# Kernel optimization log

Hardware: AMD Instinct MI355X
Metric: run time of the kernel (lower is better)

Reference implementation:

```python
import jax, jax.numpy as jnp
import numpy as np
import math

T, E = 8192, 64            # tokens, experts
K_VALUE = 2                # top-2 router
CAP_FACTOR = 1.25          # capacity_factor_train (module in training mode)
MIN_CAPACITY = 4


def _get_capacity(tokens, experts):
    cap = math.floor(K_VALUE * CAP_FACTOR * tokens / experts)
    cap += cap % 2  # make even
    cap = max(cap, MIN_CAPACITY)
    assert cap > 0
    return int(cap)


def setup_inputs() -> dict:
    key = jax.random.key(0)
    inputs = jax.random.normal(key, (T, E), dtype=jnp.float32)
    return {"inputs": inputs}


def reference(inputs):
    tokens, experts = inputs.shape
    capacity = _get_capacity(tokens, experts)  # static (shape-derived)

    probs = jax.nn.softmax(inputs, axis=-1)                       # [T, E]
    top1_idx = jnp.argmax(probs, axis=-1)                         # [T]
    mask1 = jax.nn.one_hot(top1_idx, experts, dtype=jnp.int32)    # [T, E]
    probs_except1 = jnp.where(mask1.astype(bool), -jnp.inf, probs)
    top2_idx = jnp.argmax(probs_except1, axis=-1)                 # [T]
    mask2 = jax.nn.one_hot(top2_idx, experts, dtype=jnp.int32)

    # position of each token in its expert's queue (moe_cumsum = cumsum - 1)
    rank1 = jnp.cumsum(mask1, axis=0) - 1                          # [T, E]
    rank2 = jnp.cumsum(mask2, axis=0) - 1 + jnp.sum(mask1, axis=0, keepdims=True)

    # drop tokens beyond capacity
    mask1 = mask1 * (rank1 < capacity)
    mask2 = mask2 * (rank2 < capacity)
    used_capacity = mask1.sum(axis=0) + mask2.sum(axis=0)          # [E]

    # per-token slot index (0 if dropped) and gate weight (0 if dropped)
    r1 = jnp.sum(mask1 * rank1, axis=-1)                           # [T]
    r2 = jnp.sum(mask2 * rank2, axis=-1)
    w1 = jnp.sum(mask1 * probs, axis=-1)                           # [T]
    w2 = jnp.sum(mask2 * probs, axis=-1)
    m1b = jnp.sum(mask1, axis=-1).astype(bool)                     # kept flags
    m2b = jnp.sum(mask2, axis=-1).astype(bool)

    idx = jnp.arange(tokens)
    cb_weight = jnp.zeros((tokens, experts, capacity), dtype=inputs.dtype)
    cb_weight = cb_weight.at[idx, top1_idx, r1].add(w1)
    cb_weight = cb_weight.at[idx, top2_idx, r2].add(w2)

    sec_mask = jnp.zeros((tokens, experts, capacity), dtype=bool)
    sec_mask = sec_mask.at[idx, top1_idx, r1].max(m1b)
    sec_mask = sec_mask.at[idx, top2_idx, r2].max(m2b)

    return used_capacity, cb_weight, sec_mask
```

## Files before the change

### kernel.cpp

```cpp
#include <hip/hip_runtime.h>
#include <hip/hip_bf16.h>
#include <math.h>

#define T_TOKENS 8192
#define N_EXP    64
#define CAP      320
#define ROWSZ    (N_EXP * CAP)

__global__ __launch_bounds__(256) void moe_topk_kernel(
    const float* __restrict__ in,
    int* __restrict__ top1, int* __restrict__ top2,
    float* __restrict__ w1, float* __restrict__ w2)
{
    const int lane = threadIdx.x & 63;
    const int wv   = threadIdx.x >> 6;
    const int g    = lane >> 4;
    const int sub  = lane & 15;
    const int t    = blockIdx.x * 16 + wv * 4 + g;

    const float4 xv = ((const float4*)in)[(size_t)t * 16 + sub];
    const int b0 = sub * 4;

    float v = xv.x; int idx = b0;
    if (xv.y > v) { v = xv.y; idx = b0 + 1; }
    if (xv.z > v) { v = xv.z; idx = b0 + 2; }
    if (xv.w > v) { v = xv.w; idx = b0 + 3; }
    #pragma unroll
    for (int off = 8; off; off >>= 1) {
        float vo = __shfl_xor(v, off);
        int   io = __shfl_xor(idx, off);
        if (vo > v || (vo == v && io < idx)) { v = vo; idx = io; }
    }
    const float m  = v;
    const int   i1 = idx;

    float s = expf(xv.x - m) + expf(xv.y - m) + expf(xv.z - m) + expf(xv.w - m);
    #pragma unroll
    for (int off = 8; off; off >>= 1) s += __shfl_xor(s, off);

    const float c0 = (b0     == i1) ? -INFINITY : xv.x;
    const float c1 = (b0 + 1 == i1) ? -INFINITY : xv.y;
    const float c2 = (b0 + 2 == i1) ? -INFINITY : xv.z;
    const float c3 = (b0 + 3 == i1) ? -INFINITY : xv.w;
    float v2 = c0; int idx2 = b0;
    if (c1 > v2) { v2 = c1; idx2 = b0 + 1; }
    if (c2 > v2) { v2 = c2; idx2 = b0 + 2; }
    if (c3 > v2) { v2 = c3; idx2 = b0 + 3; }
    #pragma unroll
    for (int off = 8; off; off >>= 1) {
        float vo = __shfl_xor(v2, off);
        int   io = __shfl_xor(idx2, off);
        if (vo > v2 || (vo == v2 && io < idx2)) { v2 = vo; idx2 = io; }
    }

    if (sub == 0) {
        top1[t] = i1;
        top2[t] = idx2;
        w1[t]   = 1.0f / s;
        w2[t]   = expf(v2 - m) / s;
    }
}

__global__ __launch_bounds__(1024) void moe_rank_scatter_kernel(
    const int* __restrict__ top1, const int* __restrict__ top2,
    const float* __restrict__ w1, const float* __restrict__ w2,
    float* __restrict__ out)
{
    const int e    = blockIdx.x;
    const int tid  = threadIdx.x;
    const int lane = tid & 63;
    const int wid  = tid >> 6;

    __shared__ int wsA[16], wsB[16];

    float* __restrict__ cb  = out + N_EXP;
    float* __restrict__ sec = cb + (size_t)T_TOKENS * ROWSZ;

    const int4 a1 = ((const int4*)top1)[tid * 2];
    const int4 b1 = ((const int4*)top1)[tid * 2 + 1];
    const int m0 = (a1.x == e), m1 = (a1.y == e), m2 = (a1.z == e), m3 = (a1.w == e);
    const int m4 = (b1.x == e), m5 = (b1.y == e), m6 = (b1.z == e), m7 = (b1.w == e);
    const int cnt1 = m0 + m1 + m2 + m3 + m4 + m5 + m6 + m7;

    int sc = cnt1;
    #pragma unroll
    for (int off = 1; off < 64; off <<= 1) {
        int n = __shfl_up(sc, off);
        if (lane >= off) sc += n;
    }
    if (lane == 63) wsA[wid] = sc;
    __syncthreads();
    int wbase = 0, total1 = 0;
    #pragma unroll
    for (int w = 0; w < 16; ++w) {
        const int sv = wsA[w];
        if (w < wid) wbase += sv;
        total1 += sv;
    }
    {
        int r = wbase + sc - cnt1;
        const int t0 = tid * 8;
        #define SCAT1(K, MK)                                                  \
            if (MK) {                                                         \
                if (r < CAP) {                                                \
                    const size_t o = (size_t)(t0 + K) * ROWSZ + e * CAP + r;  \
                    cb[o]  = w1[t0 + K];                                      \
                    sec[o] = 1.0f;                                            \
                }                                                             \
                ++r;                                                          \
            }
        SCAT1(0, m0) SCAT1(1, m1) SCAT1(2, m2) SCAT1(3, m3)
        SCAT1(4, m4) SCAT1(5, m5) SCAT1(6, m6) SCAT1(7, m7)
        #undef SCAT1
    }

    const int4 a2 = ((const int4*)top2)[tid * 2];
    const int4 b2 = ((const int4*)top2)[tid * 2 + 1];
    const int n0 = (a2.x == e), n1 = (a2.y == e), n2 = (a2.z == e), n3 = (a2.w == e);
    const int n4 = (b2.x == e), n5 = (b2.y == e), n6 = (b2.z == e), n7 = (b2.w == e);
    const int cnt2 = n0 + n1 + n2 + n3 + n4 + n5 + n6 + n7;

    int sc2 = cnt2;
    #pragma unroll
    for (int off = 1; off < 64; off <<= 1) {
        int n = __shfl_up(sc2, off);
        if (lane >= off) sc2 += n;
    }
    if (lane == 63) wsB[wid] = sc2;
    __syncthreads();
    int wbase2 = 0, total2 = 0;
    #pragma unroll
    for (int w = 0; w < 16; ++w) {
        const int sv = wsB[w];
        if (w < wid) wbase2 += sv;
        total2 += sv;
    }
    {
        int r = total1 + wbase2 + sc2 - cnt2;
        const int t0 = tid * 8;
        #define SCAT2(K, NK)                                                  \
            if (NK) {                                                         \
                if (r < CAP) {                                                \
                    const size_t o = (size_t)(t0 + K) * ROWSZ + e * CAP + r;  \
                    cb[o]  = w2[t0 + K];                                      \
                    sec[o] = 1.0f;                                            \
                }                                                             \
                ++r;                                                          \
            }
        SCAT2(0, n0) SCAT2(1, n1) SCAT2(2, n2) SCAT2(3, n3)
        SCAT2(4, n4) SCAT2(5, n5) SCAT2(6, n6) SCAT2(7, n7)
        #undef SCAT2
    }

    if (tid == 0) {
        const int kept1 = min(total1, CAP);
        const int kept2 = min(max(CAP - total1, 0), total2);
        out[e] = (float)(kept1 + kept2);
    }
}

extern "C" void kernel_launch(void* const* d_in, const int* in_sizes, int n_in,
                              void* d_out, int out_size, void* d_ws, size_t ws_size,
                              hipStream_t stream) {
    const float* in  = (const float*)d_in[0];
    float*       out = (float*)d_out;

    int*   top1 = (int*)d_ws;
    int*   top2 = top1 + T_TOKENS;
    float* w1   = (float*)(top2 + T_TOKENS);
    float* w2   = w1 + T_TOKENS;

    hipMemsetAsync(d_out, 0, (size_t)out_size * sizeof(float), stream);

    moe_topk_kernel<<<T_TOKENS / 16, 256, 0, stream>>>(in, top1, top2, w1, w2);
    moe_rank_scatter_kernel<<<N_EXP, 1024, 0, stream>>>(top1, top2, w1, w2, out);
}
```

Before: 231.4 us.

## Replace memset and sparse scatter with a dense vectorized fill kernel

```diff
diff --git a/kernel.cpp b/kernel.cpp
--- a/kernel.cpp
+++ b/kernel.cpp
@@ -6,11 +6,15 @@
 #define N_EXP    64
 #define CAP      320
 #define ROWSZ    (N_EXP * CAP)
+#define ROWQ     (ROWSZ / 4)
+#define CBQ4     ((unsigned)(T_TOKENS) * (unsigned)ROWQ)
+
+typedef float f32x4 __attribute__((ext_vector_type(4)));
 
 __global__ __launch_bounds__(256) void moe_topk_kernel(
     const float* __restrict__ in,
     int* __restrict__ top1, int* __restrict__ top2,
-    float* __restrict__ w1, float* __restrict__ w2)
+    float2* __restrict__ wp)
 {
     const int lane = threadIdx.x & 63;
     const int wv   = threadIdx.x >> 6;
@@ -39,13 +43,13 @@
     for (int off = 8; off; off >>= 1) s += __shfl_xor(s, off);
 
     const float c0 = (b0     == i1) ? -INFINITY : xv.x;
-    const float c1 = (b0 + 1 == i1) ? -INFINITY : xv.y;
-    const float c2 = (b0 + 2 == i1) ? -INFINITY : xv.z;
-    const float c3 = (b0 + 3 == i1) ? -INFINITY : xv.w;
+    const float c1v = (b0 + 1 == i1) ? -INFINITY : xv.y;
+    const float c2v = (b0 + 2 == i1) ? -INFINITY : xv.z;
+    const float c3v = (b0 + 3 == i1) ? -INFINITY : xv.w;
     float v2 = c0; int idx2 = b0;
-    if (c1 > v2) { v2 = c1; idx2 = b0 + 1; }
-    if (c2 > v2) { v2 = c2; idx2 = b0 + 2; }
-    if (c3 > v2) { v2 = c3; idx2 = b0 + 3; }
+    if (c1v > v2) { v2 = c1v; idx2 = b0 + 1; }
+    if (c2v > v2) { v2 = c2v; idx2 = b0 + 2; }
+    if (c3v > v2) { v2 = c3v; idx2 = b0 + 3; }
     #pragma unroll
     for (int off = 8; off; off >>= 1) {
         float vo = __shfl_xor(v2, off);
@@ -56,14 +60,13 @@
     if (sub == 0) {
         top1[t] = i1;
         top2[t] = idx2;
-        w1[t]   = 1.0f / s;
-        w2[t]   = expf(v2 - m) / s;
+        wp[t]   = make_float2(1.0f / s, expf(v2 - m) / s);
     }
 }
 
-__global__ __launch_bounds__(1024) void moe_rank_scatter_kernel(
+__global__ __launch_bounds__(1024) void moe_rank_kernel(
     const int* __restrict__ top1, const int* __restrict__ top2,
-    const float* __restrict__ w1, const float* __restrict__ w2,
+    int* __restrict__ c1, int* __restrict__ c2,
     float* __restrict__ out)
 {
     const int e    = blockIdx.x;
@@ -72,9 +75,6 @@
     const int wid  = tid >> 6;
 
     __shared__ int wsA[16], wsB[16];
-
-    float* __restrict__ cb  = out + N_EXP;
-    float* __restrict__ sec = cb + (size_t)T_TOKENS * ROWSZ;
 
     const int4 a1 = ((const int4*)top1)[tid * 2];
     const int4 b1 = ((const int4*)top1)[tid * 2 + 1];
@@ -100,18 +100,11 @@
     {
         int r = wbase + sc - cnt1;
         const int t0 = tid * 8;
-        #define SCAT1(K, MK)                                                  \
-            if (MK) {                                                         \
-                if (r < CAP) {                                                \
-                    const size_t o = (size_t)(t0 + K) * ROWSZ + e * CAP + r;  \
-                    cb[o]  = w1[t0 + K];                                      \
-                    sec[o] = 1.0f;                                            \
-                }                                                             \
-                ++r;                                                          \
-            }
-        SCAT1(0, m0) SCAT1(1, m1) SCAT1(2, m2) SCAT1(3, m3)
-        SCAT1(4, m4) SCAT1(5, m5) SCAT1(6, m6) SCAT1(7, m7)
-        #undef SCAT1
+        #define RANK1(K, MK) \
+            if (MK) { c1[t0 + K] = (r < CAP) ? (e * CAP + r) : -1; ++r; }
+        RANK1(0, m0) RANK1(1, m1) RANK1(2, m2) RANK1(3, m3)
+        RANK1(4, m4) RANK1(5, m5) RANK1(6, m6) RANK1(7, m7)
+        #undef RANK1
     }
 
     const int4 a2 = ((const int4*)top2)[tid * 2];
@@ -138,18 +131,11 @@
     {
         int r = total1 + wbase2 + sc2 - cnt2;
         const int t0 = tid * 8;
-        #define SCAT2(K, NK)                                                  \
-            if (NK) {                                                         \
-                if (r < CAP) {                                                \
-                    const size_t o = (size_t)(t0 + K) * ROWSZ + e * CAP + r;  \
-                    cb[o]  = w2[t0 + K];                                      \
-                    sec[o] = 1.0f;                                            \
-                }                                                             \
-                ++r;                                                          \
-            }
-        SCAT2(0, n0) SCAT2(1, n1) SCAT2(2, n2) SCAT2(3, n3)
-        SCAT2(4, n4) SCAT2(5, n5) SCAT2(6, n6) SCAT2(7, n7)
-        #undef SCAT2
+        #define RANK2(K, NK) \
+            if (NK) { c2[t0 + K] = (r < CAP) ? (e * CAP + r) : -1; ++r; }
+        RANK2(0, n0) RANK2(1, n1) RANK2(2, n2) RANK2(3, n3)
+        RANK2(4, n4) RANK2(5, n5) RANK2(6, n6) RANK2(7, n7)
+        #undef RANK2
     }
 
     if (tid == 0) {
@@ -159,19 +145,51 @@
     }
 }
 
+__global__ __launch_bounds__(256) void moe_fill_kernel(
+    const int* __restrict__ c1, const int* __restrict__ c2,
+    const float2* __restrict__ wp,
+    float* __restrict__ out)
+{
+    const unsigned gid = blockIdx.x * 256u + threadIdx.x;
+    const bool is_sec  = gid >= CBQ4;
+    const unsigned rq  = is_sec ? (gid - CBQ4) : gid;
+    const unsigned t   = rq / ROWQ;
+    const unsigned p   = rq % ROWQ;
+
+    const int s1 = c1[t];
+    const int s2 = c2[t];
+    float va, vb;
+    if (is_sec) { va = 1.0f; vb = 1.0f; }
+    else        { const float2 w = wp[t]; va = w.x; vb = w.y; }
+
+    const int base = (int)p * 4;
+    f32x4 v;
+    #pragma unroll
+    for (int j = 0; j < 4; ++j) {
+        const int pos = base + j;
+        float x = 0.f;
+        if (pos == s1) x += va;
+        if (pos == s2) x += vb;
+        v[j] = x;
+    }
+    ((f32x4*)(out + N_EXP))[gid] = v;
+}
+
 extern "C" void kernel_launch(void* const* d_in, const int* in_sizes, int n_in,
                               void* d_out, int out_size, void* d_ws, size_t ws_size,
                               hipStream_t stream) {
     const float* in  = (const float*)d_in[0];
     float*       out = (float*)d_out;
 
-    int*   top1 = (int*)d_ws;
-    int*   top2 = top1 + T_TOKENS;
-    float* w1   = (float*)(top2 + T_TOKENS);
-    float* w2   = w1 + T_TOKENS;
+    int*    top1 = (int*)d_ws;
+    int*    top2 = top1 + T_TOKENS;
+    int*    c1   = top2 + T_TOKENS;
+    int*    c2   = c1 + T_TOKENS;
+    float2* wp   = (float2*)(c2 + T_TOKENS);
 
-    hipMemsetAsync(d_out, 0, (size_t)out_size * sizeof(float), stream);
+    moe_topk_kernel<<<T_TOKENS / 16, 256, 0, stream>>>(in, top1, top2, wp);
+    moe_rank_kernel<<<N_EXP, 1024, 0, stream>>>(top1, top2, c1, c2, out);
 
-    moe_topk_kernel<<<T_TOKENS / 16, 256, 0, stream>>>(in, top1, top2, w1, w2);
-    moe_rank_scatter_kernel<<<N_EXP, 1024, 0, stream>>>(top1, top2, w1, w2, out);
+    const unsigned nq4 = 2u * CBQ4;
+    moe_fill_kernel<<<nq4 / 256u, 256, 0, stream>>>(c1, c2, wp, out);
 }
```

New measurement: 290.1 us. 1.25x slower.
